# Kernel tuning notes

Hardware: AMD Instinct MI355X
Metric: run time of the kernel (lower is better)

Reference implementation:

```python
import jax, jax.numpy as jnp
import numpy as np


def setup_inputs() -> dict:
    key = jax.random.key(0)
    ks = jax.random.split(key, 6)
    N, E, D = 50000, 400000, 128
    x = jax.random.normal(ks[0], (N, D), dtype=jnp.float32)
    edge_attr = jax.random.normal(ks[1], (E, D), dtype=jnp.float32)
    edge_index = jax.random.randint(ks[2], (2, E), 0, N, dtype=jnp.int64)
    # LatentMLP: two linear layers (3*D -> D -> D) with ReLU activations
    W1 = jax.random.normal(ks[3], (3 * D, D), dtype=jnp.float32) * (1.0 / np.sqrt(3 * D))
    b1 = jnp.zeros((D,), dtype=jnp.float32)
    W2 = jax.random.normal(ks[4], (D, D), dtype=jnp.float32) * (1.0 / np.sqrt(D))
    b2 = jnp.zeros((D,), dtype=jnp.float32)
    return {"x": x, "edge_attr": edge_attr, "edge_index": edge_index,
            "W1": W1, "b1": b1, "W2": W2, "b2": b2}


def reference(x, edge_attr, edge_index, W1, b1, W2, b2):
    src, dst = edge_index[0], edge_index[1]
    # gather node features per edge: [E, D] each
    agg = jnp.concatenate([x[src], x[dst], edge_attr], axis=1)  # [E, 3D]
    h = jax.nn.relu(agg @ W1 + b1)   # [E, D]
    out = jax.nn.relu(h @ W2 + b2)   # [E, D] -> new edge_attr
    return out
```

## Files before the change

### kernel.cpp

```cpp
#include <hip/hip_runtime.h>
#include <hip/hip_bf16.h>

typedef __bf16 bf16_t;
typedef __bf16 bf16x8 __attribute__((ext_vector_type(8)));
typedef __bf16 bf16x4 __attribute__((ext_vector_type(4)));
typedef float  f32x4  __attribute__((ext_vector_type(4)));

#define D 128
#define UV_LDS 131072

__device__ __forceinline__ int swz(int r, int c) {
    return (r * D + c) ^ ((r & 7) << 3);
}

__global__ void prep_weights_kernel(const float* __restrict__ W1,
                                    const float* __restrict__ W2,
                                    bf16_t* __restrict__ ws,
                                    bf16_t* __restrict__ wsf) {
    int b = blockIdx.x;
    if (b < 256) {
        int t = b * 256 + threadIdx.x;
        int s = t >> 14, r = t & 16383;
        int n = r >> 7, k = r & 127;
        float v = (s < 3) ? W1[(s * 128 + k) * 128 + n] : W2[k * 128 + n];
        ws[t] = (bf16_t)v;
    } else {
        int t = (b - 256) * 256 + threadIdx.x;
        int lane = t & 63, f = t >> 6;
        int n = f & 7, kk = (f >> 3) & 3, g = f >> 5;
        int c = n * 16 + (lane & 15);
        int k0 = kk * 32 + (lane >> 4) * 8;
        bf16x8 v;
#pragma unroll
        for (int j = 0; j < 8; j++) {
            int k = k0 + j;
            float w = (g == 0) ? W1[(256 + k) * 128 + c] : W2[k * 128 + c];
            v[j] = (bf16_t)w;
        }
        *(bf16x8*)(wsf + t * 8) = v;
    }
}

__global__ __launch_bounds__(512, 2)
void uv_kernel(const float* __restrict__ x, const bf16_t* __restrict__ ws,
               const float* __restrict__ b1, bf16_t* __restrict__ u,
               bf16_t* __restrict__ v, int N) {
    extern __shared__ __align__(16) bf16_t lds[];
    const int tid = threadIdx.x, lane = tid & 63, wv = tid >> 6;
    const int col0 = lane & 15, krow = lane >> 4, l31 = lane & 31, half = lane >> 5;
    const int gr = lane >> 4, gc = (lane & 15) * 8;
    const int n0 = blockIdx.x * 256 + wv * 32;
    bf16_t* Ach = lds + 32768 + wv * 4096;

    f32x4 xb[16];
#pragma unroll
    for (int j = 0; j < 16; j++) {
        int node = min(n0 + j * 2 + half, N - 1);
        xb[j] = *(const f32x4*)(x + (long long)node * D + l31 * 4);
    }
#pragma unroll
    for (int s = 0; s < 2; s++)
#pragma unroll
        for (int j = 0; j < 4; j++) {
            int row = j * 32 + (tid >> 4), slot = (tid & 15) * 8;
            bf16x8 w = *(const bf16x8*)(ws + s * 16384 + row * 128 + slot);
            *(bf16x8*)&lds[s * 16384 + swz(row, slot)] = w;
        }
    float bias1[8];
#pragma unroll
    for (int n = 0; n < 8; n++) bias1[n] = b1[n * 16 + col0];
#pragma unroll
    for (int j = 0; j < 16; j++) {
        f32x4 vv = xb[j];
        bf16x4 hv = { (bf16_t)vv.x, (bf16_t)vv.y, (bf16_t)vv.z, (bf16_t)vv.w };
        *(bf16x4*)&Ach[swz(j * 2 + half, l31 * 4)] = hv;
    }
    __syncthreads();

    f32x4 aU[2][8], aV[2][8];
#pragma unroll
    for (int m = 0; m < 2; m++)
#pragma unroll
        for (int n = 0; n < 8; n++) { aU[m][n] = (f32x4){0,0,0,0}; aV[m][n] = (f32x4){0,0,0,0}; }
#pragma unroll
    for (int kk = 0; kk < 4; kk++) {
        bf16x8 a0 = *(const bf16x8*)&Ach[swz(col0, kk*32 + krow*8)];
        bf16x8 a1 = *(const bf16x8*)&Ach[swz(16 + col0, kk*32 + krow*8)];
#pragma unroll
        for (int n = 0; n < 8; n++) {
            bf16x8 bU = *(const bf16x8*)&lds[swz(n*16 + col0, kk*32 + krow*8)];
            bf16x8 bV = *(const bf16x8*)&lds[16384 + swz(n*16 + col0, kk*32 + krow*8)];
            aU[0][n] = __builtin_amdgcn_mfma_f32_16x16x32_bf16(a0, bU, aU[0][n], 0,0,0);
            aU[1][n] = __builtin_amdgcn_mfma_f32_16x16x32_bf16(a1, bU, aU[1][n], 0,0,0);
            aV[0][n] = __builtin_amdgcn_mfma_f32_16x16x32_bf16(a0, bV, aV[0][n], 0,0,0);
            aV[1][n] = __builtin_amdgcn_mfma_f32_16x16x32_bf16(a1, bV, aV[1][n], 0,0,0);
        }
    }
#pragma unroll
    for (int m = 0; m < 2; m++)
#pragma unroll
        for (int n = 0; n < 8; n++)
#pragma unroll
            for (int ri = 0; ri < 4; ri++)
                Ach[swz(m*16 + krow*4 + ri, n*16 + col0)] = (bf16_t)(aU[m][n][ri] + bias1[n]);
#pragma unroll
    for (int j = 0; j < 8; j++) {
        int r = j * 4 + gr, node = n0 + r;
        if (node < N) *(bf16x8*)(u + (long long)node * D + gc) = *(const bf16x8*)&Ach[swz(r, gc)];
    }
#pragma unroll
    for (int m = 0; m < 2; m++)
#pragma unroll
        for (int n = 0; n < 8; n++)
#pragma unroll
            for (int ri = 0; ri < 4; ri++)
                Ach[swz(m*16 + krow*4 + ri, n*16 + col0)] = (bf16_t)(aV[m][n][ri]);
#pragma unroll
    for (int j = 0; j < 8; j++) {
        int r = j * 4 + gr, node = n0 + r;
        if (node < N) *(bf16x8*)(v + (long long)node * D + gc) = *(const bf16x8*)&Ach[swz(r, gc)];
    }
}

__global__ __launch_bounds__(256, 3)
void edge_kernel(const bf16_t* __restrict__ u, const bf16_t* __restrict__ v,
                 const float* __restrict__ ea, const int* __restrict__ ei,
                 const bf16_t* __restrict__ wsf, const float* __restrict__ b2,
                 float* __restrict__ out, int E) {
    __shared__ __align__(16) bf16_t Ach[2][32 * D];
    __shared__ __align__(16) bf16_t Hch[2][32 * D];

    const int tid  = threadIdx.x, lane = tid & 63, wv = tid >> 6;
    const int col0 = lane & 15, krow = lane >> 4, l31 = lane & 31;
    const int e0   = blockIdx.x * 64;

    f32x4 eaR[2][4];
#pragma unroll
    for (int c = 0; c < 2; c++)
#pragma unroll
        for (int j = 0; j < 4; j++) {
            int r = wv * 8 + j * 2 + (lane >> 5);
            int e = min(e0 + c * 32 + r, E - 1);
            eaR[c][j] = *(const f32x4*)(ea + (long long)e * D + l31 * 4);
        }
    int sidx[2], didx[2];
#pragma unroll
    for (int c = 0; c < 2; c++) {
        int er8 = min(e0 + c * 32 + wv * 8 + (lane & 7), E - 1);
        sidx[c] = ei[er8];
        didx[c] = ei[E + er8];
    }
    bf16x8 B1[4][2];
#pragma unroll
    for (int kk = 0; kk < 4; kk++)
#pragma unroll
        for (int j = 0; j < 2; j++)
            B1[kk][j] = *(const bf16x8*)(wsf + (((kk) * 8 + (wv * 2 + j)) * 64 + lane) * 8);
    float bias2[2];
    bias2[0] = b2[wv * 32 + col0];
    bias2[1] = b2[wv * 32 + 16 + col0];

#pragma unroll
    for (int c = 0; c < 2; c++)
#pragma unroll
        for (int j = 0; j < 4; j++) {
            int r = wv * 8 + j * 2 + (lane >> 5);
            f32x4 vv = eaR[c][j];
            bf16x4 hv = { (bf16_t)vv.x, (bf16_t)vv.y, (bf16_t)vv.z, (bf16_t)vv.w };
            *(bf16x4*)&Ach[c][swz(r, l31 * 4)] = hv;
        }
    __syncthreads();

    bf16x8 uR[2][2], vR[2][2];
#pragma unroll
    for (int c = 0; c < 2; c++)
#pragma unroll
        for (int j = 0; j < 2; j++) {
            int gi = __shfl(sidx[c], j * 4 + (lane >> 4));
            uR[c][j] = *(const bf16x8*)(u + (long long)gi * D + col0 * 8);
            int gj = __shfl(didx[c], j * 4 + (lane >> 4));
            vR[c][j] = *(const bf16x8*)(v + (long long)gj * D + col0 * 8);
        }
    bf16x8 B2[4][2];
#pragma unroll
    for (int kk = 0; kk < 4; kk++)
#pragma unroll
        for (int j = 0; j < 2; j++)
            B2[kk][j] = *(const bf16x8*)(wsf + (((4 + kk) * 8 + (wv * 2 + j)) * 64 + lane) * 8);

    f32x4 acc[2][2][2];
#pragma unroll
    for (int c = 0; c < 2; c++)
#pragma unroll
        for (int m = 0; m < 2; m++)
#pragma unroll
            for (int j = 0; j < 2; j++) acc[c][m][j] = (f32x4){0,0,0,0};
#pragma unroll
    for (int kk = 0; kk < 4; kk++) {
#pragma unroll
        for (int c = 0; c < 2; c++) {
            bf16x8 a0 = *(const bf16x8*)&Ach[c][swz(     col0, kk*32 + krow*8)];
            bf16x8 a1 = *(const bf16x8*)&Ach[c][swz(16 + col0, kk*32 + krow*8)];
#pragma unroll
            for (int j = 0; j < 2; j++) {
                acc[c][0][j] = __builtin_amdgcn_mfma_f32_16x16x32_bf16(a0, B1[kk][j], acc[c][0][j], 0,0,0);
                acc[c][1][j] = __builtin_amdgcn_mfma_f32_16x16x32_bf16(a1, B1[kk][j], acc[c][1][j], 0,0,0);
            }
        }
    }
#pragma unroll
    for (int c = 0; c < 2; c++)
#pragma unroll
        for (int m = 0; m < 2; m++)
#pragma unroll
            for (int j = 0; j < 2; j++)
#pragma unroll
                for (int ri = 0; ri < 4; ri++)
                    Hch[c][swz(m*16 + krow*4 + ri, wv*32 + j*16 + col0)] = (bf16_t)acc[c][m][j][ri];
    __syncthreads();

#pragma unroll
    for (int c = 0; c < 2; c++)
#pragma unroll
        for (int j = 0; j < 2; j++) {
            int r = wv * 8 + j * 4 + (lane >> 4);
            bf16x8 p8 = *(const bf16x8*)&Hch[c][swz(r, col0 * 8)];
            bf16x8 h8;
#pragma unroll
            for (int t = 0; t < 8; t++)
                h8[t] = (bf16_t)fmaxf((float)p8[t] + (float)uR[c][j][t] + (float)vR[c][j][t], 0.f);
            *(bf16x8*)&Hch[c][swz(r, col0 * 8)] = h8;
        }
    __syncthreads();

#pragma unroll
    for (int c = 0; c < 2; c++)
#pragma unroll
        for (int m = 0; m < 2; m++)
#pragma unroll
            for (int j = 0; j < 2; j++) acc[c][m][j] = (f32x4){0,0,0,0};
#pragma unroll
    for (int kk = 0; kk < 4; kk++) {
#pragma unroll
        for (int c = 0; c < 2; c++) {
            bf16x8 a0 = *(const bf16x8*)&Hch[c][swz(     col0, kk*32 + krow*8)];
            bf16x8 a1 = *(const bf16x8*)&Hch[c][swz(16 + col0, kk*32 + krow*8)];
#pragma unroll
            for (int j = 0; j < 2; j++) {
                acc[c][0][j] = __builtin_amdgcn_mfma_f32_16x16x32_bf16(a0, B2[kk][j], acc[c][0][j], 0,0,0);
                acc[c][1][j] = __builtin_amdgcn_mfma_f32_16x16x32_bf16(a1, B2[kk][j], acc[c][1][j], 0,0,0);
            }
        }
    }
#pragma unroll
    for (int c = 0; c < 2; c++)
#pragma unroll
        for (int m = 0; m < 2; m++)
#pragma unroll
            for (int j = 0; j < 2; j++)
#pragma unroll
                for (int ri = 0; ri < 4; ri++) {
                    int e = e0 + c * 32 + m*16 + krow*4 + ri;
                    if (e < E)
                        out[(long long)e * D + wv*32 + j*16 + col0] = fmaxf(acc[c][m][j][ri] + bias2[j], 0.f);
                }
}

extern "C" void kernel_launch(void* const* d_in, const int* in_sizes, int n_in,
                              void* d_out, int out_size, void* d_ws, size_t ws_size,
                              hipStream_t stream) {
    const float* x  = (const float*)d_in[0];
    const float* ea = (const float*)d_in[1];
    const int*   ei = (const int*)d_in[2];
    const float* W1 = (const float*)d_in[3];
    const float* b1 = (const float*)d_in[4];
    const float* W2 = (const float*)d_in[5];
    const float* b2 = (const float*)d_in[6];
    float* out = (float*)d_out;

    const int E = in_sizes[1] / D;
    const int N = in_sizes[0] / D;

    bf16_t* wsl = (bf16_t*)d_ws;
    bf16_t* wsf = wsl + 4 * 16384;
    bf16_t* uu  = wsf + 32768;
    bf16_t* vv  = uu + (size_t)N * D;

    prep_weights_kernel<<<272, 256, 0, stream>>>(W1, W2, wsl, wsf);

    hipFuncSetAttribute(reinterpret_cast<const void*>(uv_kernel),
                        hipFuncAttributeMaxDynamicSharedMemorySize, UV_LDS);
    uv_kernel<<<(N + 255) / 256, 512, UV_LDS, stream>>>(x, wsl, b1, uu, vv, N);

    int nblocks = (E + 63) / 64;
    edge_kernel<<<nblocks, 256, 0, stream>>>(uu, vv, ea, ei, wsf, b2, out, E);
}
```

Before: 125.0 us.

## Make edge kernel persistent with grid-stride loop and prefetch next tile's inputs

The edge kernel becomes persistent: it launches a fixed grid of 768 blocks that loop over 64-edge tiles with a grid stride. While a tile is being processed, the next tile's edge_attr rows and src/dst indices are loaded into registers. This is meant to hide global load latency and cut per-block launch and setup cost. In exchange, the weight fragments are reloaded from global or L2 every iteration, and the extra prefetch registers could lower occupancy.

```diff
diff --git a/kernel.cpp b/kernel.cpp
--- a/kernel.cpp
+++ b/kernel.cpp
@@ -132,138 +132,170 @@
 
     const int tid  = threadIdx.x, lane = tid & 63, wv = tid >> 6;
     const int col0 = lane & 15, krow = lane >> 4, l31 = lane & 31;
-    const int e0   = blockIdx.x * 64;
-
-    f32x4 eaR[2][4];
-#pragma unroll
-    for (int c = 0; c < 2; c++)
-#pragma unroll
-        for (int j = 0; j < 4; j++) {
-            int r = wv * 8 + j * 2 + (lane >> 5);
-            int e = min(e0 + c * 32 + r, E - 1);
-            eaR[c][j] = *(const f32x4*)(ea + (long long)e * D + l31 * 4);
-        }
-    int sidx[2], didx[2];
-#pragma unroll
-    for (int c = 0; c < 2; c++) {
-        int er8 = min(e0 + c * 32 + wv * 8 + (lane & 7), E - 1);
-        sidx[c] = ei[er8];
-        didx[c] = ei[E + er8];
-    }
-    bf16x8 B1[4][2];
-#pragma unroll
-    for (int kk = 0; kk < 4; kk++)
-#pragma unroll
-        for (int j = 0; j < 2; j++)
-            B1[kk][j] = *(const bf16x8*)(wsf + (((kk) * 8 + (wv * 2 + j)) * 64 + lane) * 8);
+
+    const int nst    = (E + 63) >> 6;
+    const int stride = gridDim.x;
+    int st = blockIdx.x;
+    if (st >= nst) return;
+
     float bias2[2];
     bias2[0] = b2[wv * 32 + col0];
     bias2[1] = b2[wv * 32 + 16 + col0];
 
-#pragma unroll
-    for (int c = 0; c < 2; c++)
-#pragma unroll
-        for (int j = 0; j < 4; j++) {
-            int r = wv * 8 + j * 2 + (lane >> 5);
-            f32x4 vv = eaR[c][j];
-            bf16x4 hv = { (bf16_t)vv.x, (bf16_t)vv.y, (bf16_t)vv.z, (bf16_t)vv.w };
-            *(bf16x4*)&Ach[c][swz(r, l31 * 4)] = hv;
-        }
-    __syncthreads();
-
-    bf16x8 uR[2][2], vR[2][2];
-#pragma unroll
-    for (int c = 0; c < 2; c++)
-#pragma unroll
-        for (int j = 0; j < 2; j++) {
-            int gi = __shfl(sidx[c], j * 4 + (lane >> 4));
-            uR[c][j] = *(const bf16x8*)(u + (long long)gi * D + col0 * 8);
-            int gj = __shfl(didx[c], j * 4 + (lane >> 4));
-            vR[c][j] = *(const bf16x8*)(v + (long long)gj * D + col0 * 8);
-        }
-    bf16x8 B2[4][2];
-#pragma unroll
-    for (int kk = 0; kk < 4; kk++)
-#pragma unroll
-        for (int j = 0; j < 2; j++)
-            B2[kk][j] = *(const bf16x8*)(wsf + (((4 + kk) * 8 + (wv * 2 + j)) * 64 + lane) * 8);
-
-    f32x4 acc[2][2][2];
-#pragma unroll
-    for (int c = 0; c < 2; c++)
-#pragma unroll
-        for (int m = 0; m < 2; m++)
-#pragma unroll
-            for (int j = 0; j < 2; j++) acc[c][m][j] = (f32x4){0,0,0,0};
-#pragma unroll
-    for (int kk = 0; kk < 4; kk++) {
+    f32x4 eaR[2][4];
+    int sidx[2], didx[2];
+    {
+        const int e0 = st * 64;
 #pragma unroll
         for (int c = 0; c < 2; c++) {
-            bf16x8 a0 = *(const bf16x8*)&Ach[c][swz(     col0, kk*32 + krow*8)];
-            bf16x8 a1 = *(const bf16x8*)&Ach[c][swz(16 + col0, kk*32 + krow*8)];
+#pragma unroll
+            for (int j = 0; j < 4; j++) {
+                int r = wv * 8 + j * 2 + (lane >> 5);
+                int e = min(e0 + c * 32 + r, E - 1);
+                eaR[c][j] = *(const f32x4*)(ea + (long long)e * D + l31 * 4);
+            }
+            int er8 = min(e0 + c * 32 + wv * 8 + (lane & 7), E - 1);
+            sidx[c] = ei[er8];
+            didx[c] = ei[E + er8];
+        }
+    }
+
+    for (; st < nst; st += stride) {
+        const int stn = st + stride;
+        const int e0  = st * 64;
+
+#pragma unroll
+        for (int c = 0; c < 2; c++)
+#pragma unroll
+            for (int j = 0; j < 4; j++) {
+                int r = wv * 8 + j * 2 + (lane >> 5);
+                f32x4 vv = eaR[c][j];
+                bf16x4 hv = { (bf16_t)vv.x, (bf16_t)vv.y, (bf16_t)vv.z, (bf16_t)vv.w };
+                *(bf16x4*)&Ach[c][swz(r, l31 * 4)] = hv;
+            }
+        int sidxN[2], didxN[2];
+        if (stn < nst) {
+            const int e0n = stn * 64;
+#pragma unroll
+            for (int c = 0; c < 2; c++) {
+#pragma unroll
+                for (int j = 0; j < 4; j++) {
+                    int r = wv * 8 + j * 2 + (lane >> 5);
+                    int e = min(e0n + c * 32 + r, E - 1);
+                    eaR[c][j] = *(const f32x4*)(ea + (long long)e * D + l31 * 4);
+                }
+                int er8 = min(e0n + c * 32 + wv * 8 + (lane & 7), E - 1);
+                sidxN[c] = ei[er8];
+                didxN[c] = ei[E + er8];
+            }
+        } else {
+            sidxN[0] = sidxN[1] = didxN[0] = didxN[1] = 0;
+        }
+        __syncthreads();
+
+        bf16x8 uR[2][2], vR[2][2];
+#pragma unroll
+        for (int c = 0; c < 2; c++)
 #pragma unroll
             for (int j = 0; j < 2; j++) {
-                acc[c][0][j] = __builtin_amdgcn_mfma_f32_16x16x32_bf16(a0, B1[kk][j], acc[c][0][j], 0,0,0);
-                acc[c][1][j] = __builtin_amdgcn_mfma_f32_16x16x32_bf16(a1, B1[kk][j], acc[c][1][j], 0,0,0);
-            }
-        }
-    }
-#pragma unroll
-    for (int c = 0; c < 2; c++)
-#pragma unroll
-        for (int m = 0; m < 2; m++)
+                int gi = __shfl(sidx[c], j * 4 + (lane >> 4));
+                uR[c][j] = *(const bf16x8*)(u + (long long)gi * D + col0 * 8);
+                int gj = __shfl(didx[c], j * 4 + (lane >> 4));
+                vR[c][j] = *(const bf16x8*)(v + (long long)gj * D + col0 * 8);
+            }
+        bf16x8 B1[4][2];
+#pragma unroll
+        for (int kk = 0; kk < 4; kk++)
 #pragma unroll
             for (int j = 0; j < 2; j++)
-#pragma unroll
-                for (int ri = 0; ri < 4; ri++)
-                    Hch[c][swz(m*16 + krow*4 + ri, wv*32 + j*16 + col0)] = (bf16_t)acc[c][m][j][ri];
-    __syncthreads();
-
-#pragma unroll
-    for (int c = 0; c < 2; c++)
-#pragma unroll
-        for (int j = 0; j < 2; j++) {
-            int r = wv * 8 + j * 4 + (lane >> 4);
-            bf16x8 p8 = *(const bf16x8*)&Hch[c][swz(r, col0 * 8)];
-            bf16x8 h8;
-#pragma unroll
-            for (int t = 0; t < 8; t++)
-                h8[t] = (bf16_t)fmaxf((float)p8[t] + (float)uR[c][j][t] + (float)vR[c][j][t], 0.f);
-            *(bf16x8*)&Hch[c][swz(r, col0 * 8)] = h8;
-        }
-    __syncthreads();
-
-#pragma unroll
-    for (int c = 0; c < 2; c++)
-#pragma unroll
-        for (int m = 0; m < 2; m++)
-#pragma unroll
-            for (int j = 0; j < 2; j++) acc[c][m][j] = (f32x4){0,0,0,0};
-#pragma unroll
-    for (int kk = 0; kk < 4; kk++) {
-#pragma unroll
-        for (int c = 0; c < 2; c++) {
-            bf16x8 a0 = *(const bf16x8*)&Hch[c][swz(     col0, kk*32 + krow*8)];
-            bf16x8 a1 = *(const bf16x8*)&Hch[c][swz(16 + col0, kk*32 + krow*8)];
+                B1[kk][j] = *(const bf16x8*)(wsf + (((kk) * 8 + (wv * 2 + j)) * 64 + lane) * 8);
+
+        f32x4 acc[2][2][2];
+#pragma unroll
+        for (int c = 0; c < 2; c++)
+#pragma unroll
+            for (int m = 0; m < 2; m++)
+#pragma unroll
+                for (int j = 0; j < 2; j++) acc[c][m][j] = (f32x4){0,0,0,0};
+#pragma unroll
+        for (int kk = 0; kk < 4; kk++) {
+#pragma unroll
+            for (int c = 0; c < 2; c++) {
+                bf16x8 a0 = *(const bf16x8*)&Ach[c][swz(     col0, kk*32 + krow*8)];
+                bf16x8 a1 = *(const bf16x8*)&Ach[c][swz(16 + col0, kk*32 + krow*8)];
+#pragma unroll
+                for (int j = 0; j < 2; j++) {
+                    acc[c][0][j] = __builtin_amdgcn_mfma_f32_16x16x32_bf16(a0, B1[kk][j], acc[c][0][j], 0,0,0);
+                    acc[c][1][j] = __builtin_amdgcn_mfma_f32_16x16x32_bf16(a1, B1[kk][j], acc[c][1][j], 0,0,0);
+                }
+            }
+        }
+#pragma unroll
+        for (int c = 0; c < 2; c++)
+#pragma unroll
+            for (int m = 0; m < 2; m++)
+#pragma unroll
+                for (int j = 0; j < 2; j++)
+#pragma unroll
+                    for (int ri = 0; ri < 4; ri++)
+                        Hch[c][swz(m*16 + krow*4 + ri, wv*32 + j*16 + col0)] = (bf16_t)acc[c][m][j][ri];
+        __syncthreads();
+
+#pragma unroll
+        for (int c = 0; c < 2; c++)
 #pragma unroll
             for (int j = 0; j < 2; j++) {
-                acc[c][0][j] = __builtin_amdgcn_mfma_f32_16x16x32_bf16(a0, B2[kk][j], acc[c][0][j], 0,0,0);
-                acc[c][1][j] = __builtin_amdgcn_mfma_f32_16x16x32_bf16(a1, B2[kk][j], acc[c][1][j], 0,0,0);
-            }
-        }
-    }
-#pragma unroll
-    for (int c = 0; c < 2; c++)
-#pragma unroll
-        for (int m = 0; m < 2; m++)
+                int r = wv * 8 + j * 4 + (lane >> 4);
+                bf16x8 p8 = *(const bf16x8*)&Hch[c][swz(r, col0 * 8)];
+                bf16x8 h8;
+#pragma unroll
+                for (int t = 0; t < 8; t++)
+                    h8[t] = (bf16_t)fmaxf((float)p8[t] + (float)uR[c][j][t] + (float)vR[c][j][t], 0.f);
+                *(bf16x8*)&Hch[c][swz(r, col0 * 8)] = h8;
+            }
+        __syncthreads();
+
+        bf16x8 B2[4][2];
+#pragma unroll
+        for (int kk = 0; kk < 4; kk++)
 #pragma unroll
             for (int j = 0; j < 2; j++)
-#pragma unroll
-                for (int ri = 0; ri < 4; ri++) {
-                    int e = e0 + c * 32 + m*16 + krow*4 + ri;
-                    if (e < E)
-                        out[(long long)e * D + wv*32 + j*16 + col0] = fmaxf(acc[c][m][j][ri] + bias2[j], 0.f);
+                B2[kk][j] = *(const bf16x8*)(wsf + (((4 + kk) * 8 + (wv * 2 + j)) * 64 + lane) * 8);
+#pragma unroll
+        for (int c = 0; c < 2; c++)
+#pragma unroll
+            for (int m = 0; m < 2; m++)
+#pragma unroll
+                for (int j = 0; j < 2; j++) acc[c][m][j] = (f32x4){0,0,0,0};
+#pragma unroll
+        for (int kk = 0; kk < 4; kk++) {
+#pragma unroll
+            for (int c = 0; c < 2; c++) {
+                bf16x8 a0 = *(const bf16x8*)&Hch[c][swz(     col0, kk*32 + krow*8)];
+                bf16x8 a1 = *(const bf16x8*)&Hch[c][swz(16 + col0, kk*32 + krow*8)];
+#pragma unroll
+                for (int j = 0; j < 2; j++) {
+                    acc[c][0][j] = __builtin_amdgcn_mfma_f32_16x16x32_bf16(a0, B2[kk][j], acc[c][0][j], 0,0,0);
+                    acc[c][1][j] = __builtin_amdgcn_mfma_f32_16x16x32_bf16(a1, B2[kk][j], acc[c][1][j], 0,0,0);
                 }
+            }
+        }
+#pragma unroll
+        for (int c = 0; c < 2; c++)
+#pragma unroll
+            for (int m = 0; m < 2; m++)
+#pragma unroll
+                for (int j = 0; j < 2; j++)
+#pragma unroll
+                    for (int ri = 0; ri < 4; ri++) {
+                        int e = e0 + c * 32 + m*16 + krow*4 + ri;
+                        if (e < E)
+                            out[(long long)e * D + wv*32 + j*16 + col0] = fmaxf(acc[c][m][j][ri] + bias2[j], 0.f);
+                    }
+
+        sidx[0] = sidxN[0]; sidx[1] = sidxN[1];
+        didx[0] = didxN[0]; didx[1] = didxN[1];
+    }
 }
 
 extern "C" void kernel_launch(void* const* d_in, const int* in_sizes, int n_in,
@@ -292,6 +324,5 @@
                         hipFuncAttributeMaxDynamicSharedMemorySize, UV_LDS);
     uv_kernel<<<(N + 255) / 256, 512, UV_LDS, stream>>>(x, wsl, b1, uu, vv, N);
 
-    int nblocks = (E + 63) / 64;
-    edge_kernel<<<nblocks, 256, 0, stream>>>(uu, vv, ea, ei, wsf, b2, out, E);
-}
+    edge_kernel<<<768, 256, 0, stream>>>(uu, vv, ea, ei, wsf, b2, out, E);
+}
```

After: 209.4 us. 67.5% more time.
